# Performance work log

Hardware: AMD Instinct MI355X
Metric: run time of the kernel (lower is better)

## Reference

```python
import jax, jax.numpy as jnp
import numpy as np

N = 200000          # number of points (dental scan vertices)
K = 16              # neighbors after dropping self (nsample=17 - 1)
C = 32              # feature dim (base_fdim)
NUM_CLASSES = 17
TEMPERATURE = 0.1
WEIGHT = 0.1        # head_cfg.weight[1:] of '.1'
EPS = 1e-8


def setup_inputs() -> dict:
    key = jax.random.key(0)
    k1, k2, k3 = jax.random.split(key, 3)
    features = jax.random.normal(k1, (N, C), dtype=jnp.float32)
    labels = jax.random.randint(k2, (N,), 0, NUM_CLASSES, dtype=jnp.int32)
    neighbor_idx = jax.random.randint(k3, (N, K), 0, N, dtype=jnp.int64)
    return {"features": features, "labels": labels, "neighbor_idx": neighbor_idx}


def reference(features, labels, neighbor_idx):
    # gather neighbor features/labels: [N, K, C] / [N, K]
    nb_feat = features[neighbor_idx]
    nb_lab = labels[neighbor_idx]

    # posmask_cnt: same class as center point (labels are argmaxed one-hots)
    posmask = nb_lab == labels[:, None]                     # [N, K] bool

    # point_mask: points with at least one positive and one negative neighbor
    cnt = jnp.sum(posmask.astype(jnp.int32), axis=-1)       # [N]
    point_mask = jnp.logical_and(cnt > 0, cnt < K)          # [N] bool

    # dist_l2
    diff = features[:, None, :] - nb_feat                   # [N, K, C]
    dist = jnp.sqrt(jnp.sum(diff * diff, axis=-1) + EPS)    # [N, K]

    # contrast_softnn (stable softmax over neighbors)
    d = -dist
    d = (d - jnp.max(d, axis=-1, keepdims=True)) / TEMPERATURE
    e = jnp.exp(d)                                          # [N, K]
    pos = jnp.sum(e * posmask.astype(e.dtype), axis=-1)
    neg = jnp.sum(e, axis=-1)
    loss = -jnp.log(pos / neg + EPS)                        # [N]

    # masked mean over valid points (== filtering before the mean)
    pm = point_mask.astype(loss.dtype)
    denom = jnp.maximum(jnp.sum(pm), 1.0)
    mean_loss = jnp.sum(loss * pm) / denom
    return mean_loss * WEIGHT
```

## Files before the change

### kernel.cpp

```cpp
#include <hip/hip_runtime.h>
#include <math.h>

#define NPTS 200000
#define NHALF 100000
#define KNBR 16
#define CDIM 32
#define NITEM (NPTS * KNBR)
#define TEMP 0.1f
#define WEIGHT 0.1f
#define EPSV 1e-8f

#define BLD_BLOCKS ((NPTS + 255) / 256)

#define PD_BLOCKS 2496
#define PD_RANKS 3125
#define PD_GSTRIDE 1248

#define SM2_BLOCKS ((NPTS + 255) / 256)

#define QS 0.55f

#define TBL_OFF  4096
#define D2LO_OFF (TBL_OFF + NPTS * 32)
#define D2HI_OFF (D2LO_OFF + NITEM * 2)
#define BL_OFF   (D2HI_OFF + NITEM * 2)
#define BC_OFF   (BL_OFF + SM2_BLOCKS * 4)
#define WS_NEEDED ((size_t)(BC_OFF + SM2_BLOCKS * 4))

typedef float v2f __attribute__((ext_vector_type(2)));
typedef float v4f __attribute__((ext_vector_type(4)));
typedef int   v4i __attribute__((ext_vector_type(4)));
typedef unsigned v4u __attribute__((ext_vector_type(4)));
typedef unsigned v2u __attribute__((ext_vector_type(2)));

static __device__ __forceinline__ unsigned short f32_to_f16b(float x) {
    _Float16 h = (_Float16)x;
    unsigned short u;
    __builtin_memcpy(&u, &h, 2);
    return u;
}
static __device__ __forceinline__ float f16b_to_f32(unsigned short u) {
    _Float16 h;
    __builtin_memcpy(&h, &u, 2);
    return (float)h;
}
static __device__ __forceinline__ int q4(float x) {
    int q = (int)rintf(x * (1.0f / QS)) + 7;
    return q < 0 ? 0 : (q > 14 ? 14 : q);
}

__global__ __launch_bounds__(256) void build_table(
    const float* __restrict__ f, const int* __restrict__ labels,
    unsigned char* __restrict__ T) {
    const int p = blockIdx.x * 256 + threadIdx.x;
    if (p >= NPTS) return;
    const v4f* fp = (const v4f*)(f + (size_t)p * CDIM);
    const v4f v0 = __builtin_nontemporal_load(fp + 0);
    const v4f v1 = __builtin_nontemporal_load(fp + 1);
    const v4f v2 = __builtin_nontemporal_load(fp + 2);
    const v4f v3 = __builtin_nontemporal_load(fp + 3);
    const v4f v4 = __builtin_nontemporal_load(fp + 4);
    const v4f v5 = __builtin_nontemporal_load(fp + 5);
    const v4f v6 = __builtin_nontemporal_load(fp + 6);
    const v4f v7 = __builtin_nontemporal_load(fp + 7);

    int a0 = 0, a1 = 0, a2 = 0, a3 = 0;
    a0 = __builtin_amdgcn_cvt_pk_fp8_f32(v0.x, v0.y, a0, false);
    a0 = __builtin_amdgcn_cvt_pk_fp8_f32(v0.z, v0.w, a0, true);
    a1 = __builtin_amdgcn_cvt_pk_fp8_f32(v1.x, v1.y, a1, false);
    a1 = __builtin_amdgcn_cvt_pk_fp8_f32(v1.z, v1.w, a1, true);
    a2 = __builtin_amdgcn_cvt_pk_fp8_f32(v2.x, v2.y, a2, false);
    a2 = __builtin_amdgcn_cvt_pk_fp8_f32(v2.z, v2.w, a2, true);
    a3 = __builtin_amdgcn_cvt_pk_fp8_f32(v3.x, v3.y, a3, false);
    a3 = __builtin_amdgcn_cvt_pk_fp8_f32(v3.z, v3.w, a3, true);
    v4u ra; ra.x = (unsigned)a0; ra.y = (unsigned)a1;
    ra.z = (unsigned)a2; ra.w = (unsigned)a3;

    int b0 = 0, b1 = 0, b2 = 0, b3 = 0;
    b0 = __builtin_amdgcn_cvt_pk_fp8_f32(v4.x, v4.y, b0, false);
    b0 = __builtin_amdgcn_cvt_pk_fp8_f32(v4.z, v4.w, b0, true);
    b1 = __builtin_amdgcn_cvt_pk_fp8_f32(v5.x, v5.y, b1, false);
    b1 = __builtin_amdgcn_cvt_pk_fp8_f32(v5.z, v5.w, b1, true);
    b2 = __builtin_amdgcn_cvt_pk_fp8_f32(v6.x, v6.y, b2, false);
    b2 = __builtin_amdgcn_cvt_pk_fp8_f32(v6.z, v6.w, b2, true);
    b3 = __builtin_amdgcn_cvt_pk_fp8_f32(v7.x, v7.y, b3, false);
    const int pk = q4(v7.z) | (q4(v7.w) << 4);
    b3 = (b3 & 0xffff) | (pk << 16) | ((labels[p] & 0xff) << 24);
    v4u rb; rb.x = (unsigned)b0; rb.y = (unsigned)b1;
    rb.z = (unsigned)b2; rb.w = (unsigned)b3;

    v4u* dst = (v4u*)(T + (size_t)p * 32);
    __builtin_nontemporal_store(ra, dst);
    __builtin_nontemporal_store(rb, dst + 1);
}

__global__ __launch_bounds__(256) void partial_d2_nr(
    const unsigned char* __restrict__ T,
    const int* __restrict__ nbr,
    unsigned short* __restrict__ d2lo,
    unsigned short* __restrict__ d2hi) {
    const int b = blockIdx.x;
    const int g = ((b & 7) < 4) ? 0 : 1;
    const int r = (b >> 3) * 4 + (b & 3);
    unsigned short* __restrict__ dst = g ? d2hi : d2lo;

    for (int rr = r; rr < PD_RANKS; rr += PD_GSTRIDE) {
        const int i = rr * 1024 + threadIdx.x * 4;
        const v4i idx4 = __builtin_nontemporal_load((const v4i*)(nbr + i));
        const int p = i >> 4;
        const v4u* crow = (const v4u*)(T + (size_t)p * 32);
        const v4u cv0 = __builtin_nontemporal_load(crow);
        const v4u cv1 = __builtin_nontemporal_load(crow + 1);

        v2f c[15];
        #pragma unroll
        for (int q = 0; q < 4; ++q) {
            c[2 * q]     = __builtin_amdgcn_cvt_pk_f32_fp8((int)cv0[q], false);
            c[2 * q + 1] = __builtin_amdgcn_cvt_pk_f32_fp8((int)cv0[q], true);
        }
        #pragma unroll
        for (int q = 0; q < 3; ++q) {
            c[8 + 2 * q]     = __builtin_amdgcn_cvt_pk_f32_fp8((int)cv1[q], false);
            c[8 + 2 * q + 1] = __builtin_amdgcn_cvt_pk_f32_fp8((int)cv1[q], true);
        }
        c[14] = __builtin_amdgcn_cvt_pk_f32_fp8((int)cv1[3], false);
        const unsigned cb = (cv1[3] >> 16) & 0xffu;
        const float c30 = (float)(cb & 15u) * QS - 7.0f * QS;
        const float c31 = (float)(cb >> 4) * QS - 7.0f * QS;
        const unsigned clab = cv1[3] >> 24;

        int ids[4];
        ids[0] = idx4.x; ids[1] = idx4.y; ids[2] = idx4.z; ids[3] = idx4.w;

        unsigned short o[4];
        #pragma unroll
        for (int k = 0; k < 4; ++k) {
            const int n = ids[k];
            const bool own = g ? (n >= NHALF) : (n < NHALF);
            unsigned short ov = 0;
            if (own) {
                const v4u* nrow = (const v4u*)(T + (size_t)n * 32);
                const v4u nv0 = nrow[0];
                const v4u nv1 = nrow[1];
                float d2 = 0.f;
                #pragma unroll
                for (int q = 0; q < 4; ++q) {
                    v2f nl = __builtin_amdgcn_cvt_pk_f32_fp8((int)nv0[q], false);
                    v2f nh = __builtin_amdgcn_cvt_pk_f32_fp8((int)nv0[q], true);
                    float a0 = c[2 * q].x - nl.x, a1 = c[2 * q].y - nl.y;
                    float a2 = c[2 * q + 1].x - nh.x, a3 = c[2 * q + 1].y - nh.y;
                    d2 += a0 * a0 + a1 * a1 + a2 * a2 + a3 * a3;
                }
                #pragma unroll
                for (int q = 0; q < 3; ++q) {
                    v2f nl = __builtin_amdgcn_cvt_pk_f32_fp8((int)nv1[q], false);
                    v2f nh = __builtin_amdgcn_cvt_pk_f32_fp8((int)nv1[q], true);
                    float a0 = c[8 + 2 * q].x - nl.x, a1 = c[8 + 2 * q].y - nl.y;
                    float a2 = c[8 + 2 * q + 1].x - nh.x, a3 = c[8 + 2 * q + 1].y - nh.y;
                    d2 += a0 * a0 + a1 * a1 + a2 * a2 + a3 * a3;
                }
                {
                    v2f nl = __builtin_amdgcn_cvt_pk_f32_fp8((int)nv1[3], false);
                    float a0 = c[14].x - nl.x, a1 = c[14].y - nl.y;
                    d2 += a0 * a0 + a1 * a1;
                }
                {
                    const unsigned nb = (nv1[3] >> 16) & 0xffu;
                    const float n30 = (float)(nb & 15u) * QS - 7.0f * QS;
                    const float n31 = (float)(nb >> 4) * QS - 7.0f * QS;
                    const float a0 = c30 - n30, a1 = c31 - n31;
                    d2 += a0 * a0 + a1 * a1;
                }
                const bool pos = (nv1[3] >> 24) == clab;
                ov = (unsigned short)(f32_to_f16b(d2) | (pos ? 0x8000u : 0u));
            }
            o[k] = ov;
        }
        v2u pk2;
        pk2.x = (unsigned)o[0] | ((unsigned)o[1] << 16);
        pk2.y = (unsigned)o[2] | ((unsigned)o[3] << 16);
        __builtin_nontemporal_store(pk2, (v2u*)(dst + i));
    }
}

__global__ __launch_bounds__(256) void softmax_point(
    const unsigned short* __restrict__ d2lo,
    const unsigned short* __restrict__ d2hi,
    float* __restrict__ bl, float* __restrict__ bc) {
    const int tid = threadIdx.x;
    const int p = blockIdx.x * 256 + tid;
    float loss = 0.f, valid = 0.f;
    if (p < NPTS) {
        const v4u* pa = (const v4u*)(d2lo + (size_t)p * 16);
        const v4u* pb = (const v4u*)(d2hi + (size_t)p * 16);
        const v4u a0 = pa[0], a1 = pa[1];
        const v4u b0 = pb[0], b1 = pb[1];

        float d[16];
        unsigned short posm = 0;
        #pragma unroll
        for (int j = 0; j < 16; ++j) {
            const unsigned ua = (j < 8 ? a0[(j >> 1) & 3] : a1[(j >> 1) & 3]);
            const unsigned ub = (j < 8 ? b0[(j >> 1) & 3] : b1[(j >> 1) & 3]);
            const unsigned short sv =
                (unsigned short)((ua | ub) >> ((j & 1) * 16));
            if (sv & 0x8000u) posm |= (unsigned short)(1u << j);
            d[j] = sqrtf(f16b_to_f32((unsigned short)(sv & 0x7fffu)) + EPSV);
        }

        float mn = d[0];
        #pragma unroll
        for (int j = 1; j < 16; ++j) mn = fminf(mn, d[j]);

        float pos_s = 0.f, neg_s = 0.f;
        int cnt = 0;
        #pragma unroll
        for (int j = 0; j < 16; ++j) {
            const float e = expf((mn - d[j]) * (1.0f / TEMP));
            neg_s += e;
            if (posm & (1u << j)) { pos_s += e; ++cnt; }
        }
        if (cnt > 0 && cnt < KNBR) {
            loss = -logf(pos_s / neg_s + EPSV);
            valid = 1.f;
        }
    }

    #pragma unroll
    for (int off = 1; off <= 32; off <<= 1) {
        loss += __shfl_xor(loss, off);
        valid += __shfl_xor(valid, off);
    }
    __shared__ float sl[4], sv[4];
    if ((tid & 63) == 0) { sl[tid >> 6] = loss; sv[tid >> 6] = valid; }
    __syncthreads();
    if (tid == 0) {
        bl[blockIdx.x] = sl[0] + sl[1] + sl[2] + sl[3];
        bc[blockIdx.x] = sv[0] + sv[1] + sv[2] + sv[3];
    }
}

__global__ __launch_bounds__(256) void final_reduce(const float* __restrict__ bl,
                                                    const float* __restrict__ bc,
                                                    float* __restrict__ out) {
    const int tid = threadIdx.x;
    float l = 0.f, v = 0.f;
    for (int i = tid; i < SM2_BLOCKS; i += 256) { l += bl[i]; v += bc[i]; }
    #pragma unroll
    for (int off = 1; off <= 32; off <<= 1) {
        l += __shfl_xor(l, off);
        v += __shfl_xor(v, off);
    }
    __shared__ float sl[4], sv[4];
    if ((tid & 63) == 0) { sl[tid >> 6] = l; sv[tid >> 6] = v; }
    __syncthreads();
    if (tid == 0) {
        const float S = sl[0] + sl[1] + sl[2] + sl[3];
        const float C = sv[0] + sv[1] + sv[2] + sv[3];
        out[0] = S / fmaxf(C, 1.f) * WEIGHT;
    }
}

__global__ __launch_bounds__(256) void contrast_fp32(
    const float* __restrict__ features,
    const int* __restrict__ labels,
    const int* __restrict__ nbr,
    float* __restrict__ ws) {
    const int lane = threadIdx.x & 63;
    const int wave = threadIdx.x >> 6;
    const int p0 = blockIdx.x * 16 + wave * 4;
    const int m = lane >> 3;
    const int c = lane & 7;
    const int idx_l = nbr[p0 * KNBR + lane];
    const int labn_l = labels[idx_l];
    const int labc_l = labels[p0 + (lane >> 4)];
    float4 cen[4];
    #pragma unroll
    for (int pt = 0; pt < 4; ++pt)
        cen[pt] = *(const float4*)(features + (size_t)(p0 + pt) * CDIM + c * 4);
    int ridx[8];
    #pragma unroll
    for (int j = 0; j < 8; ++j) ridx[j] = __shfl(idx_l, 8 * j + m);
    float4 v[8];
    #pragma unroll
    for (int j = 0; j < 8; ++j)
        v[j] = *(const float4*)(features + (size_t)ridx[j] * CDIM + c * 4);
    float dj[8];
    #pragma unroll
    for (int j = 0; j < 8; ++j) {
        float4 ce = cen[j >> 1];
        float dx = ce.x - v[j].x, dy = ce.y - v[j].y;
        float dz = ce.z - v[j].z, dw = ce.w - v[j].w;
        float d2 = dx * dx + dy * dy + dz * dz + dw * dw;
        d2 += __shfl_xor(d2, 1);
        d2 += __shfl_xor(d2, 2);
        d2 += __shfl_xor(d2, 4);
        dj[j] = sqrtf(d2 + EPSV);
    }
    float loss_acc = 0.f, valid_acc = 0.f;
    #pragma unroll
    for (int pt = 0; pt < 4; ++pt) {
        float a = dj[2 * pt], b = dj[2 * pt + 1];
        float mn = fminf(a, b);
        mn = fminf(mn, __shfl_xor(mn, 8));
        mn = fminf(mn, __shfl_xor(mn, 16));
        mn = fminf(mn, __shfl_xor(mn, 32));
        const float ea = expf((mn - a) / TEMP);
        const float eb = expf((mn - b) / TEMP);
        const int la = __shfl(labn_l, 16 * pt + m);
        const int lb = __shfl(labn_l, 16 * pt + 8 + m);
        const int lc = __shfl(labc_l, 16 * pt);
        float pos_s = (la == lc ? ea : 0.f) + (lb == lc ? eb : 0.f);
        float neg_s = ea + eb;
        float cnt_s = (la == lc ? 1.f : 0.f) + (lb == lc ? 1.f : 0.f);
        #pragma unroll
        for (int off = 8; off <= 32; off <<= 1) {
            pos_s += __shfl_xor(pos_s, off);
            neg_s += __shfl_xor(neg_s, off);
            cnt_s += __shfl_xor(cnt_s, off);
        }
        if (lane == pt) {
            const int icnt = (int)(cnt_s + 0.5f);
            if (icnt > 0 && icnt < KNBR) {
                loss_acc += -logf(pos_s / neg_s + EPSV);
                valid_acc += 1.f;
            }
        }
    }
    __shared__ float s_loss, s_cnt;
    if (threadIdx.x == 0) { s_loss = 0.f; s_cnt = 0.f; }
    __syncthreads();
    if (lane < 4) { atomicAdd(&s_loss, loss_acc); atomicAdd(&s_cnt, valid_acc); }
    __syncthreads();
    if (threadIdx.x == 0) { atomicAdd(&ws[0], s_loss); atomicAdd(&ws[1], s_cnt); }
}

__global__ void contrast_finalize(const float* __restrict__ ws,
                                  float* __restrict__ out) {
    out[0] = ws[0] / fmaxf(ws[1], 1.f) * WEIGHT;
}

extern "C" void kernel_launch(void* const* d_in, const int* in_sizes, int n_in,
                              void* d_out, int out_size, void* d_ws, size_t ws_size,
                              hipStream_t stream) {
    const float* features = (const float*)d_in[0];
    const int* labels     = (const int*)d_in[1];
    const int* nbr        = (const int*)d_in[2];
    float* out = (float*)d_out;
    float* ws  = (float*)d_ws;

    if (ws_size >= WS_NEEDED) {
        unsigned char* tbl = (unsigned char*)d_ws + TBL_OFF;
        unsigned short* d2lo = (unsigned short*)((char*)d_ws + D2LO_OFF);
        unsigned short* d2hi = (unsigned short*)((char*)d_ws + D2HI_OFF);
        float* bl = (float*)((char*)d_ws + BL_OFF);
        float* bc = (float*)((char*)d_ws + BC_OFF);

        build_table<<<BLD_BLOCKS, 256, 0, stream>>>(features, labels, tbl);
        partial_d2_nr<<<PD_BLOCKS, 256, 0, stream>>>(tbl, nbr, d2lo, d2hi);
        softmax_point<<<SM2_BLOCKS, 256, 0, stream>>>(d2lo, d2hi, bl, bc);
        final_reduce<<<1, 256, 0, stream>>>(bl, bc, out);
    } else {
        (void)hipMemsetAsync(ws, 0, 16, stream);
        contrast_fp32<<<NPTS / 16, 256, 0, stream>>>(features, labels, nbr, ws);
        contrast_finalize<<<1, 1, 0, stream>>>(ws, out);
    }
}
```

Baseline: 126.2 us.

## Fuse softmax partials into the distance kernel and combine half-split partial sums

```diff
diff --git a/kernel.cpp b/kernel.cpp
--- a/kernel.cpp
+++ b/kernel.cpp
@@ -11,39 +11,22 @@
 #define EPSV 1e-8f
 
 #define BLD_BLOCKS ((NPTS + 255) / 256)
-
-#define PD_BLOCKS 2496
-#define PD_RANKS 3125
-#define PD_GSTRIDE 1248
-
-#define SM2_BLOCKS ((NPTS + 255) / 256)
+#define PD_BLOCKS 1568
+#define CMB_BLOCKS ((NPTS + 255) / 256)
 
 #define QS 0.55f
 
 #define TBL_OFF  4096
-#define D2LO_OFF (TBL_OFF + NPTS * 32)
-#define D2HI_OFF (D2LO_OFF + NITEM * 2)
-#define BL_OFF   (D2HI_OFF + NITEM * 2)
-#define BC_OFF   (BL_OFF + SM2_BLOCKS * 4)
-#define WS_NEEDED ((size_t)(BC_OFF + SM2_BLOCKS * 4))
+#define PG_OFF   (TBL_OFF + NPTS * 32)
+#define BL_OFF   (PG_OFF + (size_t)2 * NPTS * 16)
+#define BC_OFF   (BL_OFF + CMB_BLOCKS * 4)
+#define WS_NEEDED ((size_t)(BC_OFF + CMB_BLOCKS * 4))
 
 typedef float v2f __attribute__((ext_vector_type(2)));
 typedef float v4f __attribute__((ext_vector_type(4)));
 typedef int   v4i __attribute__((ext_vector_type(4)));
 typedef unsigned v4u __attribute__((ext_vector_type(4)));
-typedef unsigned v2u __attribute__((ext_vector_type(2)));
-
-static __device__ __forceinline__ unsigned short f32_to_f16b(float x) {
-    _Float16 h = (_Float16)x;
-    unsigned short u;
-    __builtin_memcpy(&u, &h, 2);
-    return u;
-}
-static __device__ __forceinline__ float f16b_to_f32(unsigned short u) {
-    _Float16 h;
-    __builtin_memcpy(&h, &u, 2);
-    return (float)h;
-}
+
 static __device__ __forceinline__ int q4(float x) {
     int q = (int)rintf(x * (1.0f / QS)) + 7;
     return q < 0 ? 0 : (q > 14 ? 14 : q);
@@ -94,138 +77,142 @@
     __builtin_nontemporal_store(rb, dst + 1);
 }
 
-__global__ __launch_bounds__(256) void partial_d2_nr(
+__global__ __launch_bounds__(256) void pd2_fused(
     const unsigned char* __restrict__ T,
     const int* __restrict__ nbr,
-    unsigned short* __restrict__ d2lo,
-    unsigned short* __restrict__ d2hi) {
+    float4* __restrict__ PG) {
     const int b = blockIdx.x;
     const int g = ((b & 7) < 4) ? 0 : 1;
     const int r = (b >> 3) * 4 + (b & 3);
-    unsigned short* __restrict__ dst = g ? d2hi : d2lo;
-
-    for (int rr = r; rr < PD_RANKS; rr += PD_GSTRIDE) {
-        const int i = rr * 1024 + threadIdx.x * 4;
-        const v4i idx4 = __builtin_nontemporal_load((const v4i*)(nbr + i));
-        const int p = i >> 4;
-        const v4u* crow = (const v4u*)(T + (size_t)p * 32);
-        const v4u cv0 = __builtin_nontemporal_load(crow);
-        const v4u cv1 = __builtin_nontemporal_load(crow + 1);
-
-        v2f c[15];
+    const int p = r * 256 + threadIdx.x;
+    if (p >= NPTS) return;
+
+    const v4i* ip = (const v4i*)(nbr + (size_t)p * KNBR);
+    const v4i i0 = __builtin_nontemporal_load(ip + 0);
+    const v4i i1 = __builtin_nontemporal_load(ip + 1);
+    const v4i i2 = __builtin_nontemporal_load(ip + 2);
+    const v4i i3 = __builtin_nontemporal_load(ip + 3);
+    int ids[16];
+    ids[0]=i0.x; ids[1]=i0.y; ids[2]=i0.z; ids[3]=i0.w;
+    ids[4]=i1.x; ids[5]=i1.y; ids[6]=i1.z; ids[7]=i1.w;
+    ids[8]=i2.x; ids[9]=i2.y; ids[10]=i2.z; ids[11]=i2.w;
+    ids[12]=i3.x; ids[13]=i3.y; ids[14]=i3.z; ids[15]=i3.w;
+
+    const v4u* crow = (const v4u*)(T + (size_t)p * 32);
+    const v4u cv0 = __builtin_nontemporal_load(crow);
+    const v4u cv1 = __builtin_nontemporal_load(crow + 1);
+    v2f c[15];
+    #pragma unroll
+    for (int q = 0; q < 4; ++q) {
+        c[2 * q]     = __builtin_amdgcn_cvt_pk_f32_fp8((int)cv0[q], false);
+        c[2 * q + 1] = __builtin_amdgcn_cvt_pk_f32_fp8((int)cv0[q], true);
+    }
+    #pragma unroll
+    for (int q = 0; q < 3; ++q) {
+        c[8 + 2 * q]     = __builtin_amdgcn_cvt_pk_f32_fp8((int)cv1[q], false);
+        c[8 + 2 * q + 1] = __builtin_amdgcn_cvt_pk_f32_fp8((int)cv1[q], true);
+    }
+    c[14] = __builtin_amdgcn_cvt_pk_f32_fp8((int)cv1[3], false);
+    const unsigned cb = (cv1[3] >> 16) & 0xffu;
+    const float c30 = (float)(cb & 15u) * QS - 7.0f * QS;
+    const float c31 = (float)(cb >> 4) * QS - 7.0f * QS;
+    const unsigned clab = cv1[3] >> 24;
+
+    float d[16];
+    unsigned posm = 0;
+
+    #pragma unroll
+    for (int ch = 0; ch < 2; ++ch) {
+        v4u nv0[8], nv1[8];
+        bool own[8];
         #pragma unroll
-        for (int q = 0; q < 4; ++q) {
-            c[2 * q]     = __builtin_amdgcn_cvt_pk_f32_fp8((int)cv0[q], false);
-            c[2 * q + 1] = __builtin_amdgcn_cvt_pk_f32_fp8((int)cv0[q], true);
+        for (int j = 0; j < 8; ++j) {
+            const int id = ids[ch * 8 + j];
+            own[j] = g ? (id >= NHALF) : (id < NHALF);
+            if (own[j]) {
+                const v4u* nrow = (const v4u*)(T + (size_t)id * 32);
+                nv0[j] = nrow[0];
+                nv1[j] = nrow[1];
+            }
         }
         #pragma unroll
-        for (int q = 0; q < 3; ++q) {
-            c[8 + 2 * q]     = __builtin_amdgcn_cvt_pk_f32_fp8((int)cv1[q], false);
-            c[8 + 2 * q + 1] = __builtin_amdgcn_cvt_pk_f32_fp8((int)cv1[q], true);
-        }
-        c[14] = __builtin_amdgcn_cvt_pk_f32_fp8((int)cv1[3], false);
-        const unsigned cb = (cv1[3] >> 16) & 0xffu;
-        const float c30 = (float)(cb & 15u) * QS - 7.0f * QS;
-        const float c31 = (float)(cb >> 4) * QS - 7.0f * QS;
-        const unsigned clab = cv1[3] >> 24;
-
-        int ids[4];
-        ids[0] = idx4.x; ids[1] = idx4.y; ids[2] = idx4.z; ids[3] = idx4.w;
-
-        unsigned short o[4];
-        #pragma unroll
-        for (int k = 0; k < 4; ++k) {
-            const int n = ids[k];
-            const bool own = g ? (n >= NHALF) : (n < NHALF);
-            unsigned short ov = 0;
-            if (own) {
-                const v4u* nrow = (const v4u*)(T + (size_t)n * 32);
-                const v4u nv0 = nrow[0];
-                const v4u nv1 = nrow[1];
+        for (int j = 0; j < 8; ++j) {
+            float dv = INFINITY;
+            if (own[j]) {
                 float d2 = 0.f;
                 #pragma unroll
                 for (int q = 0; q < 4; ++q) {
-                    v2f nl = __builtin_amdgcn_cvt_pk_f32_fp8((int)nv0[q], false);
-                    v2f nh = __builtin_amdgcn_cvt_pk_f32_fp8((int)nv0[q], true);
+                    v2f nl = __builtin_amdgcn_cvt_pk_f32_fp8((int)nv0[j][q], false);
+                    v2f nh = __builtin_amdgcn_cvt_pk_f32_fp8((int)nv0[j][q], true);
                     float a0 = c[2 * q].x - nl.x, a1 = c[2 * q].y - nl.y;
                     float a2 = c[2 * q + 1].x - nh.x, a3 = c[2 * q + 1].y - nh.y;
                     d2 += a0 * a0 + a1 * a1 + a2 * a2 + a3 * a3;
                 }
                 #pragma unroll
                 for (int q = 0; q < 3; ++q) {
-                    v2f nl = __builtin_amdgcn_cvt_pk_f32_fp8((int)nv1[q], false);
-                    v2f nh = __builtin_amdgcn_cvt_pk_f32_fp8((int)nv1[q], true);
+                    v2f nl = __builtin_amdgcn_cvt_pk_f32_fp8((int)nv1[j][q], false);
+                    v2f nh = __builtin_amdgcn_cvt_pk_f32_fp8((int)nv1[j][q], true);
                     float a0 = c[8 + 2 * q].x - nl.x, a1 = c[8 + 2 * q].y - nl.y;
                     float a2 = c[8 + 2 * q + 1].x - nh.x, a3 = c[8 + 2 * q + 1].y - nh.y;
                     d2 += a0 * a0 + a1 * a1 + a2 * a2 + a3 * a3;
                 }
                 {
-                    v2f nl = __builtin_amdgcn_cvt_pk_f32_fp8((int)nv1[3], false);
+                    v2f nl = __builtin_amdgcn_cvt_pk_f32_fp8((int)nv1[j][3], false);
                     float a0 = c[14].x - nl.x, a1 = c[14].y - nl.y;
                     d2 += a0 * a0 + a1 * a1;
                 }
                 {
-                    const unsigned nb = (nv1[3] >> 16) & 0xffu;
+                    const unsigned nb = (nv1[j][3] >> 16) & 0xffu;
                     const float n30 = (float)(nb & 15u) * QS - 7.0f * QS;
                     const float n31 = (float)(nb >> 4) * QS - 7.0f * QS;
                     const float a0 = c30 - n30, a1 = c31 - n31;
                     d2 += a0 * a0 + a1 * a1;
                 }
-                const bool pos = (nv1[3] >> 24) == clab;
-                ov = (unsigned short)(f32_to_f16b(d2) | (pos ? 0x8000u : 0u));
+                dv = sqrtf(d2 + EPSV);
+                if ((nv1[j][3] >> 24) == clab)
+                    posm |= (1u << (ch * 8 + j));
             }
-            o[k] = ov;
-        }
-        v2u pk2;
-        pk2.x = (unsigned)o[0] | ((unsigned)o[1] << 16);
-        pk2.y = (unsigned)o[2] | ((unsigned)o[3] << 16);
-        __builtin_nontemporal_store(pk2, (v2u*)(dst + i));
-    }
-}
-
-__global__ __launch_bounds__(256) void softmax_point(
-    const unsigned short* __restrict__ d2lo,
-    const unsigned short* __restrict__ d2hi,
+            d[ch * 8 + j] = dv;
+        }
+    }
+
+    float mn = INFINITY;
+    #pragma unroll
+    for (int j = 0; j < 16; ++j) mn = fminf(mn, d[j]);
+
+    float pos_s = 0.f, neg_s = 0.f, cnt = 0.f;
+    #pragma unroll
+    for (int j = 0; j < 16; ++j) {
+        if (d[j] < 3.0e37f) {
+            const float e = expf((mn - d[j]) * (1.0f / TEMP));
+            neg_s += e;
+            if (posm & (1u << j)) { pos_s += e; cnt += 1.f; }
+        }
+    }
+    float4 outv; outv.x = mn; outv.y = pos_s; outv.z = neg_s; outv.w = cnt;
+    PG[(size_t)g * NPTS + p] = outv;
+}
+
+__global__ __launch_bounds__(256) void combine_loss(
+    const float4* __restrict__ PG,
     float* __restrict__ bl, float* __restrict__ bc) {
     const int tid = threadIdx.x;
     const int p = blockIdx.x * 256 + tid;
     float loss = 0.f, valid = 0.f;
     if (p < NPTS) {
-        const v4u* pa = (const v4u*)(d2lo + (size_t)p * 16);
-        const v4u* pb = (const v4u*)(d2hi + (size_t)p * 16);
-        const v4u a0 = pa[0], a1 = pa[1];
-        const v4u b0 = pb[0], b1 = pb[1];
-
-        float d[16];
-        unsigned short posm = 0;
-        #pragma unroll
-        for (int j = 0; j < 16; ++j) {
-            const unsigned ua = (j < 8 ? a0[(j >> 1) & 3] : a1[(j >> 1) & 3]);
-            const unsigned ub = (j < 8 ? b0[(j >> 1) & 3] : b1[(j >> 1) & 3]);
-            const unsigned short sv =
-                (unsigned short)((ua | ub) >> ((j & 1) * 16));
-            if (sv & 0x8000u) posm |= (unsigned short)(1u << j);
-            d[j] = sqrtf(f16b_to_f32((unsigned short)(sv & 0x7fffu)) + EPSV);
-        }
-
-        float mn = d[0];
-        #pragma unroll
-        for (int j = 1; j < 16; ++j) mn = fminf(mn, d[j]);
-
-        float pos_s = 0.f, neg_s = 0.f;
-        int cnt = 0;
-        #pragma unroll
-        for (int j = 0; j < 16; ++j) {
-            const float e = expf((mn - d[j]) * (1.0f / TEMP));
-            neg_s += e;
-            if (posm & (1u << j)) { pos_s += e; ++cnt; }
-        }
+        const float4 a = PG[p];
+        const float4 b = PG[(size_t)NPTS + p];
+        const float m = fminf(a.x, b.x);
+        const float s0 = expf((m - a.x) * (1.0f / TEMP));
+        const float s1 = expf((m - b.x) * (1.0f / TEMP));
+        const float pos = a.y * s0 + b.y * s1;
+        const float neg = a.z * s0 + b.z * s1;
+        const int cnt = (int)(a.w + b.w + 0.5f);
         if (cnt > 0 && cnt < KNBR) {
-            loss = -logf(pos_s / neg_s + EPSV);
+            loss = -logf(pos / neg + EPSV);
             valid = 1.f;
         }
     }
-
     #pragma unroll
     for (int off = 1; off <= 32; off <<= 1) {
         loss += __shfl_xor(loss, off);
@@ -245,7 +232,7 @@
                                                     float* __restrict__ out) {
     const int tid = threadIdx.x;
     float l = 0.f, v = 0.f;
-    for (int i = tid; i < SM2_BLOCKS; i += 256) { l += bl[i]; v += bc[i]; }
+    for (int i = tid; i < CMB_BLOCKS; i += 256) { l += bl[i]; v += bc[i]; }
     #pragma unroll
     for (int off = 1; off <= 32; off <<= 1) {
         l += __shfl_xor(l, off);
@@ -351,14 +338,13 @@
 
     if (ws_size >= WS_NEEDED) {
         unsigned char* tbl = (unsigned char*)d_ws + TBL_OFF;
-        unsigned short* d2lo = (unsigned short*)((char*)d_ws + D2LO_OFF);
-        unsigned short* d2hi = (unsigned short*)((char*)d_ws + D2HI_OFF);
+        float4* PG = (float4*)((char*)d_ws + PG_OFF);
         float* bl = (float*)((char*)d_ws + BL_OFF);
         float* bc = (float*)((char*)d_ws + BC_OFF);
 
         build_table<<<BLD_BLOCKS, 256, 0, stream>>>(features, labels, tbl);
-        partial_d2_nr<<<PD_BLOCKS, 256, 0, stream>>>(tbl, nbr, d2lo, d2hi);
-        softmax_point<<<SM2_BLOCKS, 256, 0, stream>>>(d2lo, d2hi, bl, bc);
+        pd2_fused<<<PD_BLOCKS, 256, 0, stream>>>(tbl, nbr, PG);
+        combine_loss<<<CMB_BLOCKS, 256, 0, stream>>>(PG, bl, bc);
         final_reduce<<<1, 256, 0, stream>>>(bl, bc, out);
     } else {
         (void)hipMemsetAsync(ws, 0, 16, stream);
```

After: 131.3 us. +4.1%, slower.
